# Kernel optimization log

Measured on AMD Instinct MI355X. Metric: run time of the kernel, lower is better.

The kernel has to match this reference:

```python
import math
import jax, jax.numpy as jnp
import numpy as np

RM = 100.0      # r_max
RN = 1000       # r_dsc
LMAX = 2
MATCH_FRAC = 0.1
PARA1 = 1.0
RD = RM / RN    # radial step
NE = 4096       # batch of trial energies


def setup_inputs() -> dict:
    key = jax.random.key(0)
    # small negative energies (bound-state regime) to keep the exponential
    # Numerov growth over 900 steps within fp32 range
    init_energy = -(jax.random.uniform(key, (NE,), dtype=jnp.float32) * 0.01 + 0.005)
    return {"init_energy": init_energy}


def _disc_solve(sol0, factor, limit):
    # sol0: (5, n_e, L) initial 5-point window; factor: (rn, n_e, L)
    # Numerov-style 4-step recurrence, vectorized coefficients + lax.scan
    c = 3.0 / 40.0 * RD ** 2
    idx = jnp.arange(1, limit - 5)
    f0 = factor[idx]
    f1 = factor[idx + 1]
    f2 = factor[idx + 2]
    f3 = factor[idx + 3]
    f4 = factor[idx + 4]
    denom = 1.0 - c * f4
    a = -1.0 + c * f0 / denom
    b = 2.0 + (13.0 / 15.0) * RD ** 2 * f1 / denom
    cc = -2.0 + (7.0 / 60.0) * RD ** 2 * f2 / denom
    d = 2.0 + (13.0 / 15.0) * RD ** 2 * f3 / denom

    def step(prev, coef):
        ca, cb, ccc, cd = coef
        new4 = ca * prev[1] + cb * prev[2] + ccc * prev[3] + cd * prev[4]
        new = jnp.concatenate([prev[1:], new4[None]], axis=0)  # shift window
        return new, new

    _, rest = jax.lax.scan(step, sol0, (a, b, cc, d))
    return jnp.concatenate([sol0[None], rest], axis=0)  # (limit-5, 5, n_e, L)


def _derivative(func, at):
    return (25.0 * func[at - 1] - 48.0 * func[at - 2] + 36.0 * func[at - 3]
            - 16.0 * func[at - 4] + 3.0 * func[at - 5]) / (12.0 * RD)


def _integrate(func):
    # faithful to original: integrand squares `func` again (func is u**2 here)
    M = func.shape[0] // 4 - 1
    g0 = func[0:4 * M:4]
    g1 = func[1:4 * M:4]
    g2 = func[2:4 * M:4]
    g3 = func[3:4 * M:4]
    g4 = func[4::4][:M]
    integrand = (7.0 * (g0 ** 2 + g4 ** 2) + 32.0 * (g1 ** 2 + g3 ** 2)
                 + 12.0 * g2) * (2.0 * RD / 45.0)
    return integrand.sum(axis=0)


def _forward(init_energy):
    L = LMAX + 1
    dt = init_energy.dtype
    n_e = init_energy.shape[0]
    r = jnp.linspace(RM / RN, RM, RN, dtype=dt).reshape(RN, 1, 1)
    l = jnp.arange(L, dtype=dt).reshape(1, 1, L)

    energy = jnp.broadcast_to(init_energy[:, None], (n_e, L))  # (n_e, L)
    e_val = energy[None]                                       # (1, n_e, L)
    # coulomb potential -1/r; factor: (rn, n_e, L)
    factor = l * (l + 1) / r ** 2 + PARA1 * (-e_val - 1.0 / r)

    # left (r->0) initial window: u ~ r^(l+1) + r^(l+2)/(2(l+1)) * (-para_1)
    r0 = jnp.linspace(RD, 5 * RD, 5, dtype=dt).reshape(5, 1, 1)
    u_zero_init = jnp.broadcast_to(
        r0 ** (l + 1) - r0 ** (l + 2) / (2.0 * (l + 1)) * PARA1, (5, n_e, L))

    # right (r->r_max) initial window: r * truncated spherical-bessel series
    r_inf = jnp.linspace(RM - 4 * RD, RM, 5, dtype=dt).reshape(5, 1, 1)
    fact = jnp.array([math.prod([2 * li + 1 for li in range(lm + 1)])
                      for lm in range(L)], dtype=dt)  # [1, 3, 15]
    x = r_inf * jnp.sqrt(jnp.abs(e_val))              # (5, n_e, L)
    base = x ** l / fact
    t1 = x ** 2 / 2.0 / (2 * l + 3)
    t2 = (x ** 2 / 2.0) ** 2 / (2.0 * (2 * l + 3) * (2 * l + 5))
    u_infty_init = jnp.broadcast_to(r_inf * (base * (1.0 + t1 + t2)), (5, n_e, L))

    match = int(RN * MATCH_FRAC)  # 100
    uz = _disc_solve(u_zero_init, factor, match)                     # (95, 5, n_e, L)
    ui = _disc_solve(u_infty_init, factor[::-1], RN - match)[::-1]   # (895, 5, n_e, L)
    u_zero = jnp.concatenate([uz[0], uz[:, 4]], axis=0)    # (100, n_e, L)
    u_infty = jnp.concatenate([ui[0], ui[:, 4]], axis=0)   # (900, n_e, L)

    lfunc_in = _derivative(u_zero, match) / u_zero[-1]
    # faithful: the trailing flip acts on the energy axis of the (n_e, L) result
    lfunc_out = _derivative(u_infty[::-1], RN - match)[::-1] / u_infty[0]
    integ_in = _integrate(u_zero ** 2)
    integ_out = _integrate(u_infty ** 2)
    delta = -(lfunc_out - lfunc_in) / (integ_in / u_zero[-1] ** 2
                                       + integ_out / u_infty[0] ** 2)
    return (energy + delta, u_zero, u_infty)


def reference(init_energy):
    return _forward(init_energy)
```

## Files before the change

kernel.cpp:

```cpp
#include <hip/hip_runtime.h>


namespace {
constexpr int kNE    = 4096;
constexpr int kNCH   = kNE * 3;
constexpr int kMatch = 100;
constexpr float kC   = 3.0f / 40.0f * 0.01f;
constexpr float kK1  = 13.0f / 15.0f * 0.01f;
constexpr float kK2  = 7.0f / 60.0f * 0.01f;
constexpr int kSeg        = 16;
constexpr int kCPB        = 32;
constexpr int kZeroBlocks = kNCH / 512;
constexpr int kInfBlocks  = kNCH / kCPB;
}

__device__ __forceinline__ float rcp_f(float x) { return __builtin_amdgcn_rcpf(x); }
__device__ __forceinline__ float rcp_nr(float x) {
    float r = __builtin_amdgcn_rcpf(x);
    return fmaf(fmaf(-x, r, 1.0f), r, r);
}

__global__ __launch_bounds__(512) void solve_kernel(const float* __restrict__ energy,
                                                    float* __restrict__ out,
                                                    float* __restrict__ ws)
{
    __shared__ float gt[899 * 3];
    __shared__ float sPT[16][15][kCPB];
    __shared__ float sSt[kSeg][4][kCPB];
    float* sR4 = &sPT[0][0][0];
    float* sR2 = sR4 + kSeg * kCPB;

    const int bid = (int)blockIdx.x;
    const int tid = (int)threadIdx.x;
    float* uzero = out + kNCH;
    float* uinf  = out + kNCH + (size_t)kMatch * kNCH;

    if (bid < kZeroBlocks) {
        const int t  = bid * 512 + tid;
        const int l  = t % 3;
        const int ei = t / 3;
        const float e = energy[ei], negE = -e;
        const float ll1 = (float)(l * (l + 1));
        const float rdiv = (l == 0) ? 0.5f : ((l == 1) ? 0.25f : (1.0f/6.0f));
        float p0,p1,p2,p3,p4;
        {
            float pw[5];
            #pragma unroll
            for (int k = 0; k < 5; ++k) {
                float r = 0.1f * (float)(k + 1);
                float rl1 = (l == 0) ? r : ((l == 1) ? r*r : r*r*r);
                pw[k] = rl1 - (rl1 * r) * rdiv;
                uzero[(size_t)k * kNCH + t] = pw[k];
            }
            uzero[(size_t)5 * kNCH + t] = pw[4];
            p0=pw[0]; p1=pw[1]; p2=pw[2]; p3=pw[3]; p4=pw[4];
        }
        float acc4, acc2;
        {
            float q0=p0*p0, q1=p1*p1, q2=p2*p2, q3=p3*p3, q4=p4*p4;
            acc4 = 7.0f*q0*q0 + 32.0f*q1*q1 + 32.0f*q3*q3 + 14.0f*q4*q4 + 32.0f*q4*q4;
            acc2 = q2;
        }
        float f0, f1, f2, f3;
        {
            float i1 = rcp_f(0.2f), i2 = rcp_f(0.3f), i3 = rcp_f(0.4f), i4 = rcp_f(0.5f);
            f0 = fmaf(i1, fmaf(ll1, i1, -1.0f), negE);
            f1 = fmaf(i2, fmaf(ll1, i2, -1.0f), negE);
            f2 = fmaf(i3, fmaf(ll1, i3, -1.0f), negE);
            f3 = fmaf(i4, fmaf(ll1, i4, -1.0f), negE);
        }
        float* ptr = uzero + (size_t)6 * kNCH + t;
        #pragma unroll 4
        for (int j = 5; j <= 98; ++j) {
            float ri = rcp_f(fmaf((float)j, 0.1f, 0.1f));
            float f4 = fmaf(ri, fmaf(ll1, ri, -1.0f), negE);
            float iv = rcp_f(fmaf(-kC, f4, 1.0f));
            float a  = fmaf(kC  * f0, iv, -1.0f);
            float b  = fmaf(kK1 * f1, iv,  2.0f);
            float cc = fmaf(kK2 * f2, iv, -2.0f);
            float d  = fmaf(kK1 * f3, iv,  2.0f);
            float nw = fmaf(d, p4, fmaf(cc, p3, fmaf(b, p2, a * p1)));
            *ptr = nw; ptr += kNCH;
            float v2 = nw*nw, v4 = v2*v2;
            if (j <= 94) {
                int m = (j + 1) & 3;
                if (m == 2)      acc2 += v2;
                else if (m == 0) acc4 += 14.0f * v4;
                else             acc4 += 32.0f * v4;
            } else if (j == 95) {
                acc4 += 7.0f * v4;
            }
            f0 = f1; f1 = f2; f2 = f3; f3 = f4;
            p0 = p1; p1 = p2; p2 = p3; p3 = p4; p4 = nw;
        }
        float integ = fmaf(12.0f, acc2, acc4) * (2.0f * 0.1f / 45.0f);
        float deriv = fmaf(25.0f, p4, fmaf(-48.0f, p3, fmaf(36.0f, p2,
                      fmaf(-16.0f, p1, 3.0f * p0)))) * (1.0f / 1.2f);
        ws[2 * kNCH + t] = deriv / p4;
        ws[3 * kNCH + t] = integ / (p4 * p4);
        return;
    }

    for (int jj = tid; jj < 899; jj += 512) {
        float ri = rcp_nr(fmaf((float)jj, -0.1f, 100.0f));
        gt[jj * 3 + 0] = -ri;
        gt[jj * 3 + 1] = ri * fmaf(2.0f, ri, -1.0f);
        gt[jj * 3 + 2] = ri * fmaf(6.0f, ri, -1.0f);
    }
    __syncthreads();

    const int b = bid - kZeroBlocks;
    const int g = tid & 31;
    const int s = tid >> 5;
    const int t = b * kCPB + g;
    const int l  = t % 3;
    const int ei = t / 3;
    const float e = energy[ei], negE = -e;
    const int jstart = (s < 15) ? (5 + 56 * s) : 843;

    const float ff0 = gt[(jstart - 4) * 3 + l] + negE;
    const float ff1 = gt[(jstart - 3) * 3 + l] + negE;
    const float ff2 = gt[(jstart - 2) * 3 + l] + negE;
    const float ff3 = gt[(jstart - 1) * 3 + l] + negE;
    float F0 = ff0, F1 = ff1, F2 = ff2, F3 = ff3;
    const float* gp0 = &gt[jstart * 3 + l];
    const float* gp = gp0;

    float ca, cb, cc_, cd;
#define COEF(FA,FB,FC,FD) \
    { float f4 = *gp + negE; gp += 3; \
      float x  = kC * f4; \
      float iv = fmaf(x, x, x) + 1.0f; \
      ca  = fmaf(kC  * FA, iv, -1.0f); \
      cb  = fmaf(kK1 * FB, iv,  2.0f); \
      cc_ = fmaf(kK2 * FC, iv, -2.0f); \
      cd  = fmaf(kK1 * FD, iv,  2.0f); \
      FA = f4; }

#define MSTEP(FA,FB,FC,FD,RA,RB,RC,RD) \
    { COEF(FA,FB,FC,FD) \
      RA[0] = fmaf(cd,RD[0], fmaf(cc_,RC[0], fmaf(cb,RB[0], ca*RA[0]))); \
      RA[1] = fmaf(cd,RD[1], fmaf(cc_,RC[1], fmaf(cb,RB[1], ca*RA[1]))); \
      RA[2] = fmaf(cd,RD[2], fmaf(cc_,RC[2], fmaf(cb,RB[2], ca*RA[2]))); \
      RA[3] = fmaf(cd,RD[3], fmaf(cc_,RC[3], fmaf(cb,RB[3], ca*RA[3]))); }

    if (s < 14) {
        float ra[4] = {1,0,0,0}, rb[4] = {0,1,0,0}, rc[4] = {0,0,1,0}, rd[4] = {0,0,0,1};
        for (int it = 0; it < 14; ++it) {
            MSTEP(F0,F1,F2,F3, ra,rb,rc,rd)
            MSTEP(F1,F2,F3,F0, rb,rc,rd,ra)
            MSTEP(F2,F3,F0,F1, rc,rd,ra,rb)
            MSTEP(F3,F0,F1,F2, rd,ra,rb,rc)
        }
        #pragma unroll
        for (int c = 0; c < 4; ++c) {
            sPT[ 0+c][s][g] = ra[c]; sPT[ 4+c][s][g] = rb[c];
            sPT[ 8+c][s][g] = rc[c]; sPT[12+c][s][g] = rd[c];
        }
    } else if (s == 14) {
        float ra[4] = {1,0,0,0}, rb[4] = {0,1,0,0}, rc[4] = {0,0,1,0}, rd[4] = {0,0,0,1};
        for (int it = 0; it < 13; ++it) {
            MSTEP(F0,F1,F2,F3, ra,rb,rc,rd)
            MSTEP(F1,F2,F3,F0, rb,rc,rd,ra)
            MSTEP(F2,F3,F0,F1, rc,rd,ra,rb)
            MSTEP(F3,F0,F1,F2, rd,ra,rb,rc)
        }
        MSTEP(F0,F1,F2,F3, ra,rb,rc,rd)
        MSTEP(F1,F2,F3,F0, rb,rc,rd,ra)
        #pragma unroll
        for (int c = 0; c < 4; ++c) {
            sPT[ 0+c][s][g] = rc[c]; sPT[ 4+c][s][g] = rd[c];
            sPT[ 8+c][s][g] = ra[c]; sPT[12+c][s][g] = rb[c];
        }
    }
    __syncthreads();

    if (s == 0) {
        const float se  = sqrtf(fabsf(e));
        const float rfc = (l == 0) ? 1.0f : ((l == 1) ? (1.0f/3.0f) : (1.0f/15.0f));
        const float rt1 = (l == 0) ? (1.0f/3.0f) : ((l == 1) ? (1.0f/5.0f) : (1.0f/7.0f));
        const float rt2 = (l == 0) ? (1.0f/30.0f) : ((l == 1) ? (1.0f/70.0f) : (1.0f/126.0f));
        float pw[5];
        #pragma unroll
        for (int k = 0; k < 5; ++k) {
            float rinf = 99.6f + 0.1f * (float)k;
            float x  = rinf * se;
            float xl = (l == 0) ? 1.0f : ((l == 1) ? x : x * x);
            float h  = x * x * 0.5f;
            pw[k] = rinf * (xl * rfc * (1.0f + h * rt1 + (h * h) * rt2));
        }
        uinf[(size_t)899 * kNCH + t] = pw[4];
        float st0 = pw[1], st1 = pw[2], st2 = pw[3], st3 = pw[4];
        for (int ss = 0; ss < kSeg; ++ss) {
            sSt[ss][0][g] = st0; sSt[ss][1][g] = st1;
            sSt[ss][2][g] = st2; sSt[ss][3][g] = st3;
            if (ss < kSeg - 1) {
                float n0 = fmaf(sPT[ 3][ss][g],st3, fmaf(sPT[ 2][ss][g],st2,
                           fmaf(sPT[ 1][ss][g],st1, sPT[ 0][ss][g]*st0)));
                float n1 = fmaf(sPT[ 7][ss][g],st3, fmaf(sPT[ 6][ss][g],st2,
                           fmaf(sPT[ 5][ss][g],st1, sPT[ 4][ss][g]*st0)));
                float n2 = fmaf(sPT[11][ss][g],st3, fmaf(sPT[10][ss][g],st2,
                           fmaf(sPT[ 9][ss][g],st1, sPT[ 8][ss][g]*st0)));
                float n3 = fmaf(sPT[15][ss][g],st3, fmaf(sPT[14][ss][g],st2,
                           fmaf(sPT[13][ss][g],st1, sPT[12][ss][g]*st0)));
                st0 = n0; st1 = n1; st2 = n2; st3 = n3;
            }
        }
    }
    __syncthreads();

    float W0[4] = {0.0f, 32.0f, 14.0f, 32.0f};
    float V0[4] = {1.0f, 0.0f, 0.0f, 0.0f};
    float WR[4] = {0.0f, 32.0f, 14.0f, 32.0f};
    float VR[4] = {1.0f, 0.0f, 0.0f, 0.0f};
    if (s == 0) {
        W0[0]=0; V0[0]=0; W0[1]=0; V0[1]=0; W0[2]=7.0f; V0[2]=0; W0[3]=32.0f; V0[3]=0;
    } else if (s == 15) {
        WR[0]=14.0f; VR[0]=0; WR[1]=32.0f; VR[1]=0; WR[2]=0; VR[2]=1.0f; WR[3]=32.0f; VR[3]=0;
        W0[0]=0; V0[0]=0; W0[1]=0; V0[1]=0; W0[2]=0; V0[2]=1.0f; W0[3]=32.0f; V0[3]=0;
    }

    gp = gp0;
    F0 = ff0; F1 = ff1; F2 = ff2; F3 = ff3;
    float p0 = sSt[s][0][g], p1 = sSt[s][1][g], p2 = sSt[s][2][g], p3 = sSt[s][3][g];
    float acc4 = 0.0f, acc2 = 0.0f;
    float* ptr = uinf + (size_t)(903 - jstart) * kNCH + t;
#define RSTEPW(FA,FB,FC,FD,PA,PB,PC,PD,W,V,K) \
    { COEF(FA,FB,FC,FD) \
      float nw = fmaf(cd,PD, fmaf(cc_,PC, fmaf(cb,PB, ca*PA))); \
      PA = nw; *ptr = nw; ptr -= kNCH; \
      float v2 = nw*nw, v4 = v2*v2; \
      acc4 = fmaf(W[K], v4, acc4); \
      acc2 = fmaf(V[K], v2, acc2); }
#define GROUP(W,V) \
    RSTEPW(F0,F1,F2,F3, p0,p1,p2,p3, W,V,0) \
    RSTEPW(F1,F2,F3,F0, p1,p2,p3,p0, W,V,1) \
    RSTEPW(F2,F3,F0,F1, p2,p3,p0,p1, W,V,2) \
    RSTEPW(F3,F0,F1,F2, p3,p0,p1,p2, W,V,3)

    GROUP(W0,V0)
    for (int it = 0; it < 12; ++it) { GROUP(WR,VR) }
    float h0 = p3;
    GROUP(WR,VR)
#undef GROUP
#undef RSTEPW

    sR4[s * kCPB + g] = acc4;
    sR2[s * kCPB + g] = acc2;
    __syncthreads();

    if (s == kSeg - 1) {
        float a4 = 0.0f, a2 = 0.0f;
        #pragma unroll
        for (int ss = 0; ss < kSeg; ++ss) {
            a4 += sR4[ss * kCPB + g]; a2 += sR2[ss * kCPB + g];
        }
        float h1 = p0, h2 = p1, h3 = p2, h4 = p3;
        uinf[(size_t)0 * kNCH + t] = h0;
        uinf[(size_t)1 * kNCH + t] = h1;
        uinf[(size_t)2 * kNCH + t] = h2;
        uinf[(size_t)3 * kNCH + t] = h3;
        uinf[(size_t)4 * kNCH + t] = h4;
        float q0 = h0*h0, q1 = h1*h1, q2 = h2*h2, q3 = h3*h3, q4 = h4*h4;
        a4 += 7.0f*q0*q0 + 32.0f*q1*q1 + 32.0f*q3*q3 + 14.0f*q4*q4;
        a2 += q2;
        float integ = fmaf(12.0f, a2, a4) * (2.0f * 0.1f / 45.0f);
        float deriv = fmaf(25.0f, h0, fmaf(-48.0f, h1, fmaf(36.0f, h2,
                      fmaf(-16.0f, h3, 3.0f * h4)))) * (1.0f / 1.2f);
        ws[t]        = deriv / h0;
        ws[kNCH + t] = integ / (h0 * h0);
    }
#undef MSTEP
#undef COEF
}

__global__ __launch_bounds__(256) void final_kernel(const float* __restrict__ energy,
                                                    const float* __restrict__ ws,
                                                    float* __restrict__ out)
{
    int t = (int)blockIdx.x * 256 + (int)threadIdx.x;
    if (t >= kNCH) return;
    int l = t % 3, ei = t / 3;
    float lf_out = ws[(kNE - 1 - ei) * 3 + l];
    float lf_in  = ws[2 * kNCH + t];
    float den    = ws[kNCH + t] + ws[3 * kNCH + t];
    out[t] = energy[ei] - (lf_out - lf_in) / den;
}

extern "C" void kernel_launch(void* const* d_in, const int* in_sizes, int n_in,
                              void* d_out, int out_size, void* d_ws, size_t ws_size,
                              hipStream_t stream) {
    (void)in_sizes; (void)n_in; (void)out_size; (void)ws_size;
    const float* energy = (const float*)d_in[0];
    float* out = (float*)d_out;
    float* ws  = (float*)d_ws;
    solve_kernel<<<kZeroBlocks + kInfBlocks, 512, 0, stream>>>(energy, out, ws);
    final_kernel<<<kNCH / 256, 256, 0, stream>>>(energy, ws, out);
}
```

Before: 88.12 us.

## Split the inward recurrence into 32 segments of 16 channels each

Each block now handles 16 channels split into 32 segments of 28 steps instead of 32 channels split into 16 segments of 56 steps. This halves the serial transfer-matrix and replay chain per thread and doubles the number of blocks. The shared table shrinks to a single 1/r array, and the potential factor is recomputed per step with FMAs. Matrices and states are stored as float4 in a combined shared buffer, which reduces LDS size, and launch bounds now request higher occupancy. The cost is a longer serial state-propagation chain for segment 0 (32 steps) and extra per-step arithmetic.

```diff
diff --git a/kernel.cpp b/kernel.cpp
--- a/kernel.cpp
+++ b/kernel.cpp
@@ -8,8 +8,8 @@
 constexpr float kC   = 3.0f / 40.0f * 0.01f;
 constexpr float kK1  = 13.0f / 15.0f * 0.01f;
 constexpr float kK2  = 7.0f / 60.0f * 0.01f;
-constexpr int kSeg        = 16;
-constexpr int kCPB        = 32;
+constexpr int kSeg        = 32;
+constexpr int kCPB        = 16;
 constexpr int kZeroBlocks = kNCH / 512;
 constexpr int kInfBlocks  = kNCH / kCPB;
 }
@@ -20,15 +20,13 @@
     return fmaf(fmaf(-x, r, 1.0f), r, r);
 }
 
-__global__ __launch_bounds__(512) void solve_kernel(const float* __restrict__ energy,
-                                                    float* __restrict__ out,
-                                                    float* __restrict__ ws)
+__global__ __launch_bounds__(512, 6) void solve_kernel(const float* __restrict__ energy,
+                                                       float* __restrict__ out,
+                                                       float* __restrict__ ws)
 {
-    __shared__ float gt[899 * 3];
-    __shared__ float sPT[16][15][kCPB];
-    __shared__ float sSt[kSeg][4][kCPB];
-    float* sR4 = &sPT[0][0][0];
-    float* sR2 = sR4 + kSeg * kCPB;
+    __shared__ float gt[899];
+    __shared__ float sM[kSeg][4][kCPB][4];
+    float* sF = &sM[0][0][0][0];
 
     const int bid = (int)blockIdx.x;
     const int tid = (int)threadIdx.x;
@@ -101,34 +99,37 @@
         return;
     }
 
-    for (int jj = tid; jj < 899; jj += 512) {
-        float ri = rcp_nr(fmaf((float)jj, -0.1f, 100.0f));
-        gt[jj * 3 + 0] = -ri;
-        gt[jj * 3 + 1] = ri * fmaf(2.0f, ri, -1.0f);
-        gt[jj * 3 + 2] = ri * fmaf(6.0f, ri, -1.0f);
-    }
+    for (int jj = tid; jj < 899; jj += 512)
+        gt[jj] = rcp_nr(fmaf((float)jj, -0.1f, 100.0f));
     __syncthreads();
 
     const int b = bid - kZeroBlocks;
-    const int g = tid & 31;
-    const int s = tid >> 5;
+    const int g = tid & (kCPB - 1);
+    const int s = tid >> 4;
     const int t = b * kCPB + g;
     const int l  = t % 3;
     const int ei = t / 3;
     const float e = energy[ei], negE = -e;
-    const int jstart = (s < 15) ? (5 + 56 * s) : 843;
-
-    const float ff0 = gt[(jstart - 4) * 3 + l] + negE;
-    const float ff1 = gt[(jstart - 3) * 3 + l] + negE;
-    const float ff2 = gt[(jstart - 2) * 3 + l] + negE;
-    const float ff3 = gt[(jstart - 1) * 3 + l] + negE;
+    const float ll1 = (float)(l * (l + 1));
+    const int jstart = (s <= 29) ? (5 + 28 * s) : ((s == 30) ? 843 : 871);
+
+    float ff0, ff1, ff2, ff3;
+    {
+        float r0 = gt[jstart - 4], r1 = gt[jstart - 3];
+        float r2 = gt[jstart - 2], r3 = gt[jstart - 1];
+        ff0 = fmaf(r0, fmaf(ll1, r0, -1.0f), negE);
+        ff1 = fmaf(r1, fmaf(ll1, r1, -1.0f), negE);
+        ff2 = fmaf(r2, fmaf(ll1, r2, -1.0f), negE);
+        ff3 = fmaf(r3, fmaf(ll1, r3, -1.0f), negE);
+    }
     float F0 = ff0, F1 = ff1, F2 = ff2, F3 = ff3;
-    const float* gp0 = &gt[jstart * 3 + l];
+    const float* gp0 = &gt[jstart];
     const float* gp = gp0;
 
     float ca, cb, cc_, cd;
 #define COEF(FA,FB,FC,FD) \
-    { float f4 = *gp + negE; gp += 3; \
+    { float ri = *gp; gp += 1; \
+      float f4 = fmaf(ri, fmaf(ll1, ri, -1.0f), negE); \
       float x  = kC * f4; \
       float iv = fmaf(x, x, x) + 1.0f; \
       ca  = fmaf(kC  * FA, iv, -1.0f); \
@@ -144,34 +145,28 @@
       RA[2] = fmaf(cd,RD[2], fmaf(cc_,RC[2], fmaf(cb,RB[2], ca*RA[2]))); \
       RA[3] = fmaf(cd,RD[3], fmaf(cc_,RC[3], fmaf(cb,RB[3], ca*RA[3]))); }
 
-    if (s < 14) {
+    if (s != 31) {
         float ra[4] = {1,0,0,0}, rb[4] = {0,1,0,0}, rc[4] = {0,0,1,0}, rd[4] = {0,0,0,1};
-        for (int it = 0; it < 14; ++it) {
+        const int full = (s == 29) ? 6 : 7;
+        for (int it = 0; it < full; ++it) {
             MSTEP(F0,F1,F2,F3, ra,rb,rc,rd)
             MSTEP(F1,F2,F3,F0, rb,rc,rd,ra)
             MSTEP(F2,F3,F0,F1, rc,rd,ra,rb)
             MSTEP(F3,F0,F1,F2, rd,ra,rb,rc)
         }
-        #pragma unroll
-        for (int c = 0; c < 4; ++c) {
-            sPT[ 0+c][s][g] = ra[c]; sPT[ 4+c][s][g] = rb[c];
-            sPT[ 8+c][s][g] = rc[c]; sPT[12+c][s][g] = rd[c];
-        }
-    } else if (s == 14) {
-        float ra[4] = {1,0,0,0}, rb[4] = {0,1,0,0}, rc[4] = {0,0,1,0}, rd[4] = {0,0,0,1};
-        for (int it = 0; it < 13; ++it) {
+        if (s == 29) {
             MSTEP(F0,F1,F2,F3, ra,rb,rc,rd)
             MSTEP(F1,F2,F3,F0, rb,rc,rd,ra)
-            MSTEP(F2,F3,F0,F1, rc,rd,ra,rb)
-            MSTEP(F3,F0,F1,F2, rd,ra,rb,rc)
-        }
-        MSTEP(F0,F1,F2,F3, ra,rb,rc,rd)
-        MSTEP(F1,F2,F3,F0, rb,rc,rd,ra)
-        #pragma unroll
-        for (int c = 0; c < 4; ++c) {
-            sPT[ 0+c][s][g] = rc[c]; sPT[ 4+c][s][g] = rd[c];
-            sPT[ 8+c][s][g] = ra[c]; sPT[12+c][s][g] = rb[c];
-        }
+            #pragma unroll
+            for (int c = 0; c < 4; ++c) {
+                float t0 = ra[c]; ra[c] = rc[c]; rc[c] = t0;
+                float t1 = rb[c]; rb[c] = rd[c]; rd[c] = t1;
+            }
+        }
+        *(float4*)&sM[s][0][g][0] = make_float4(ra[0], ra[1], ra[2], ra[3]);
+        *(float4*)&sM[s][1][g][0] = make_float4(rb[0], rb[1], rb[2], rb[3]);
+        *(float4*)&sM[s][2][g][0] = make_float4(rc[0], rc[1], rc[2], rc[3]);
+        *(float4*)&sM[s][3][g][0] = make_float4(rd[0], rd[1], rd[2], rd[3]);
     }
     __syncthreads();
 
@@ -192,18 +187,19 @@
         uinf[(size_t)899 * kNCH + t] = pw[4];
         float st0 = pw[1], st1 = pw[2], st2 = pw[3], st3 = pw[4];
         for (int ss = 0; ss < kSeg; ++ss) {
-            sSt[ss][0][g] = st0; sSt[ss][1][g] = st1;
-            sSt[ss][2][g] = st2; sSt[ss][3][g] = st3;
             if (ss < kSeg - 1) {
-                float n0 = fmaf(sPT[ 3][ss][g],st3, fmaf(sPT[ 2][ss][g],st2,
-                           fmaf(sPT[ 1][ss][g],st1, sPT[ 0][ss][g]*st0)));
-                float n1 = fmaf(sPT[ 7][ss][g],st3, fmaf(sPT[ 6][ss][g],st2,
-                           fmaf(sPT[ 5][ss][g],st1, sPT[ 4][ss][g]*st0)));
-                float n2 = fmaf(sPT[11][ss][g],st3, fmaf(sPT[10][ss][g],st2,
-                           fmaf(sPT[ 9][ss][g],st1, sPT[ 8][ss][g]*st0)));
-                float n3 = fmaf(sPT[15][ss][g],st3, fmaf(sPT[14][ss][g],st2,
-                           fmaf(sPT[13][ss][g],st1, sPT[12][ss][g]*st0)));
+                float4 M0 = *(const float4*)&sM[ss][0][g][0];
+                float4 M1 = *(const float4*)&sM[ss][1][g][0];
+                float4 M2 = *(const float4*)&sM[ss][2][g][0];
+                float4 M3 = *(const float4*)&sM[ss][3][g][0];
+                *(float4*)&sM[ss][0][g][0] = make_float4(st0, st1, st2, st3);
+                float n0 = fmaf(M0.w,st3, fmaf(M0.z,st2, fmaf(M0.y,st1, M0.x*st0)));
+                float n1 = fmaf(M1.w,st3, fmaf(M1.z,st2, fmaf(M1.y,st1, M1.x*st0)));
+                float n2 = fmaf(M2.w,st3, fmaf(M2.z,st2, fmaf(M2.y,st1, M2.x*st0)));
+                float n3 = fmaf(M3.w,st3, fmaf(M3.z,st2, fmaf(M3.y,st1, M3.x*st0)));
                 st0 = n0; st1 = n1; st2 = n2; st3 = n3;
+            } else {
+                *(float4*)&sM[ss][0][g][0] = make_float4(st0, st1, st2, st3);
             }
         }
     }
@@ -215,14 +211,24 @@
     float VR[4] = {1.0f, 0.0f, 0.0f, 0.0f};
     if (s == 0) {
         W0[0]=0; V0[0]=0; W0[1]=0; V0[1]=0; W0[2]=7.0f; V0[2]=0; W0[3]=32.0f; V0[3]=0;
-    } else if (s == 15) {
+    } else if (s >= 30) {
         WR[0]=14.0f; VR[0]=0; WR[1]=32.0f; VR[1]=0; WR[2]=0; VR[2]=1.0f; WR[3]=32.0f; VR[3]=0;
-        W0[0]=0; V0[0]=0; W0[1]=0; V0[1]=0; W0[2]=0; V0[2]=1.0f; W0[3]=32.0f; V0[3]=0;
+        if (s == 30) {
+            W0[0]=0; W0[1]=0; W0[2]=0;     W0[3]=32.0f;
+            V0[0]=0; V0[1]=0; V0[2]=1.0f;  V0[3]=0;
+        } else {
+            W0[0]=14.0f; W0[1]=32.0f; W0[2]=0;    W0[3]=32.0f;
+            V0[0]=0;     V0[1]=0;     V0[2]=1.0f; V0[3]=0;
+        }
     }
 
     gp = gp0;
     F0 = ff0; F1 = ff1; F2 = ff2; F3 = ff3;
-    float p0 = sSt[s][0][g], p1 = sSt[s][1][g], p2 = sSt[s][2][g], p3 = sSt[s][3][g];
+    float p0, p1, p2, p3;
+    {
+        float4 P = *(const float4*)&sM[s][0][g][0];
+        p0 = P.x; p1 = P.y; p2 = P.z; p3 = P.w;
+    }
     float acc4 = 0.0f, acc2 = 0.0f;
     float* ptr = uinf + (size_t)(903 - jstart) * kNCH + t;
 #define RSTEPW(FA,FB,FC,FD,PA,PB,PC,PD,W,V,K) \
@@ -239,21 +245,24 @@
     RSTEPW(F3,F0,F1,F2, p3,p0,p1,p2, W,V,3)
 
     GROUP(W0,V0)
-    for (int it = 0; it < 12; ++it) { GROUP(WR,VR) }
+    for (int it = 0; it < 5; ++it) { GROUP(WR,VR) }
     float h0 = p3;
     GROUP(WR,VR)
 #undef GROUP
 #undef RSTEPW
 
-    sR4[s * kCPB + g] = acc4;
-    sR2[s * kCPB + g] = acc2;
+    {
+        float2 rr; rr.x = acc4; rr.y = acc2;
+        *(float2*)&sF[s * 256 + 64 + 4 * g] = rr;
+    }
     __syncthreads();
 
     if (s == kSeg - 1) {
         float a4 = 0.0f, a2 = 0.0f;
         #pragma unroll
         for (int ss = 0; ss < kSeg; ++ss) {
-            a4 += sR4[ss * kCPB + g]; a2 += sR2[ss * kCPB + g];
+            float2 rr = *(const float2*)&sF[ss * 256 + 64 + 4 * g];
+            a4 += rr.x; a2 += rr.y;
         }
         float h1 = p0, h2 = p1, h3 = p2, h4 = p3;
         uinf[(size_t)0 * kNCH + t] = h0;
```

After: 86.53 us. Within noise of the previous version (-1.8%).
